# Optimization experiments

Measured on AMD Instinct MI355X. Metric: run time of the kernel, lower is better.

## Reference

```python
import jax, jax.numpy as jnp
import numpy as np

N = 100000
E = 500000
LATENT = 256
EDGE_DIM = 128
HIDDEN = 2 * EDGE_DIM  # 256


def setup_inputs() -> dict:
    key = jax.random.key(0)
    k_z, k_e, k_w1, k_b1, k_w2, k_b2 = jax.random.split(key, 6)
    z = jax.random.normal(k_z, (N, LATENT), dtype=jnp.float32)
    edge_index = jax.random.randint(k_e, (2, E), 0, N, dtype=jnp.int64)
    # torch nn.Linear init: U(-1/sqrt(fan_in), 1/sqrt(fan_in))
    lim1 = 1.0 / np.sqrt(2 * LATENT)
    W1 = jax.random.uniform(k_w1, (HIDDEN, 2 * LATENT), jnp.float32, -lim1, lim1)
    b1 = jax.random.uniform(k_b1, (HIDDEN,), jnp.float32, -lim1, lim1)
    lim2 = 1.0 / np.sqrt(HIDDEN)
    W2 = jax.random.uniform(k_w2, (EDGE_DIM, HIDDEN), jnp.float32, -lim2, lim2)
    b2 = jax.random.uniform(k_b2, (EDGE_DIM,), jnp.float32, -lim2, lim2)
    return {"z": z, "edge_index": edge_index, "W1": W1, "b1": b1, "W2": W2, "b2": b2}


def reference(z, edge_index, W1, b1, W2, b2):
    # Gather endpoint embeddings and concat: [E, 2*latent]
    src = z[edge_index[0]]
    dst = z[edge_index[1]]
    pair = jnp.concatenate([src, dst], axis=1)
    # 2-layer MLP (dropout is identity in eval mode)
    h = jax.nn.relu(pair @ W1.T + b1)
    out = h @ W2.T + b2  # [E, edge_dim]
    return out
```

## Files before the change

kernel.cpp:

```cpp
#include <hip/hip_runtime.h>
#include <hip/hip_bf16.h>

#define N_NODES 100000
#define N_EDGES 500000

typedef __attribute__((ext_vector_type(8))) short  short8;
typedef __attribute__((ext_vector_type(4))) short  short4v;
typedef __attribute__((ext_vector_type(4))) float  float4v;

__device__ __forceinline__ unsigned short f2bf(float f) {
    union { float f; unsigned int u; } v; v.f = f;
    unsigned int u = v.u;
    unsigned int r = u + 0x7fffu + ((u >> 16) & 1u);
    return (unsigned short)(r >> 16);
}
__device__ __forceinline__ float bf2f(unsigned short b) {
    union { unsigned int u; float f; } v; v.u = ((unsigned int)b) << 16;
    return v.f;
}

__device__ __forceinline__ void gload_lds16(const unsigned short* g, unsigned short* l) {
    __builtin_amdgcn_global_load_lds(
        (const __attribute__((address_space(1))) unsigned int*)g,
        (__attribute__((address_space(3))) unsigned int*)l, 16, 0, 0);
}

__global__ void zconv_kernel(const float* __restrict__ z, unsigned short* __restrict__ zb) {
    size_t i = ((size_t)blockIdx.x * 256 + threadIdx.x) * 8;
    float4v a = *(const float4v*)(z + i);
    float4v b = *(const float4v*)(z + i + 4);
    short8 o;
    o[0] = (short)f2bf(a.x); o[1] = (short)f2bf(a.y); o[2] = (short)f2bf(a.z); o[3] = (short)f2bf(a.w);
    o[4] = (short)f2bf(b.x); o[5] = (short)f2bf(b.y); o[6] = (short)f2bf(b.z); o[7] = (short)f2bf(b.w);
    *(short8*)(zb + i) = o;
}

__global__ void prep_kernel(const float* __restrict__ W1, const float* __restrict__ W2,
                            unsigned short* __restrict__ w1c, unsigned short* __restrict__ w2b) {
    int j = blockIdx.x, k = threadIdx.x;
    if (j < 512) {
        float v = (j < 256) ? W1[(size_t)j * 512 + k] : W1[(size_t)(j - 256) * 512 + 256 + k];
        w1c[(size_t)j * 256 + k] = f2bf(v);
    } else {
        int o = j - 512;
        w2b[(size_t)o * 256 + k] = f2bf(W2[(size_t)o * 256 + k]);
    }
}

__launch_bounds__(256, 2)
__global__ void stage1_kernel(const unsigned short* __restrict__ zb,
                              const unsigned short* __restrict__ w1c,
                              unsigned short* __restrict__ ZW) {
    __shared__ unsigned short lds[128 * 136];
    unsigned short* At = lds;
    unsigned short* Bt = lds + 128 * 64;

    const int t    = threadIdx.x;
    const int lane = t & 63, wave = t >> 6;
    const int wm = wave >> 1, wn = wave & 1;
    const int l15 = lane & 15, quad = lane >> 4;
    const int mbase = blockIdx.x * 128, nbase = blockIdx.y * 128;

    const int lr = lane >> 3;
    const int cg = (lane & 7) ^ lr;
    const unsigned short* ag[4]; const unsigned short* bg[4];
    unsigned short* al[4]; unsigned short* bl[4];
#pragma unroll
    for (int q = 0; q < 4; ++q) {
        int rA = wave * 32 + q * 8 + lr;
        int gA = mbase + rA; if (gA >= N_NODES) gA = N_NODES - 1;
        ag[q] = zb  + (size_t)gA * 256 + cg * 8;
        bg[q] = w1c + (size_t)(nbase + rA) * 256 + cg * 8;
        al[q] = At + (wave * 4 + q) * 512 + lane * 8;
        bl[q] = Bt + (wave * 4 + q) * 512 + lane * 8;
    }

    float4v acc[4][4];
    const float4v fz = {0.f, 0.f, 0.f, 0.f};
#pragma unroll
    for (int i = 0; i < 4; ++i)
#pragma unroll
        for (int j = 0; j < 4; ++j) acc[i][j] = fz;

    for (int kk = 0; kk < 256; kk += 64) {
        __syncthreads();
#pragma unroll
        for (int q = 0; q < 4; ++q) gload_lds16(ag[q] + kk, al[q]);
#pragma unroll
        for (int q = 0; q < 4; ++q) gload_lds16(bg[q] + kk, bl[q]);
        __syncthreads();

#pragma unroll
        for (int s = 0; s < 2; ++s) {
            const int ch = ((s * 4 + quad) ^ (l15 & 7)) * 8;
            short8 af[4], bfr[4];
#pragma unroll
            for (int i = 0; i < 4; ++i)
                af[i] = *(const short8*)(At + (wm * 64 + i * 16 + l15) * 64 + ch);
#pragma unroll
            for (int j = 0; j < 4; ++j)
                bfr[j] = *(const short8*)(Bt + (wn * 64 + j * 16 + l15) * 64 + ch);
#pragma unroll
            for (int i = 0; i < 4; ++i)
#pragma unroll
                for (int j = 0; j < 4; ++j)
                    acc[i][j] = __builtin_amdgcn_mfma_f32_16x16x32_bf16(af[i], bfr[j], acc[i][j], 0, 0, 0);
        }
    }

    __syncthreads();
#pragma unroll
    for (int i = 0; i < 4; ++i)
#pragma unroll
        for (int j = 0; j < 4; ++j) {
            int row = wm * 64 + i * 16 + quad * 4;
            int col = wn * 64 + j * 16 + l15;
#pragma unroll
            for (int r = 0; r < 4; ++r)
                lds[(row + r) * 136 + col] = f2bf(acc[i][j][r]);
        }
    __syncthreads();
    for (int c = t; c < 128 * 16; c += 256) {
        int row = c >> 4, ch2 = c & 15;
        int grow = mbase + row;
        if (grow < N_NODES)
            *(short8*)(ZW + (size_t)grow * 512 + nbase + ch2 * 8) =
                *(const short8*)(lds + row * 136 + ch2 * 8);
    }
}

#define H_PITCH 264
#define EBLK 64
__launch_bounds__(256, 4)
__global__ void stage2_kernel(const int* __restrict__ eidx, const unsigned short* __restrict__ ZW,
                              const float* __restrict__ b1, const unsigned short* __restrict__ w2b,
                              const float* __restrict__ b2, float* __restrict__ out) {
    __shared__ unsigned short h[EBLK * H_PITCH];
    __shared__ int idx[128];
    float* hf = (float*)h;
    const int t    = threadIdx.x;
    const int lane = t & 63, wave = t >> 6;
    const int l15 = lane & 15, quad = lane >> 4;
    const int wm = wave >> 1, wn = wave & 1;
    const int eb = blockIdx.x * EBLK;

    if (t < 128) {
        int e = eb + (t & 63); if (e >= N_EDGES) e = N_EDGES - 1;
        idx[t] = eidx[(t >> 6) * N_EDGES + e];
    }
    __syncthreads();

    const int lj = t & 31, er = t >> 5;
    float4v b1a = *(const float4v*)(b1 + lj * 8);
    float4v b1b = *(const float4v*)(b1 + lj * 8 + 4);
    const unsigned short* zs = ZW + lj * 8;
    const unsigned short* zd = ZW + 256 + lj * 8;

    short8 va[8], vb[8];
#pragma unroll
    for (int p = 0; p < 8; ++p) {
        int el = p * 8 + er;
        va[p] = *(const short8*)(zs + (size_t)idx[el] * 512);
        vb[p] = *(const short8*)(zd + (size_t)idx[64 + el] * 512);
    }
#pragma unroll
    for (int p = 0; p < 8; ++p) {
        int el = p * 8 + er;
        short8 xa = va[p], xb = vb[p];
        short8 rv;
#pragma unroll
        for (int i = 0; i < 8; ++i) {
            float v = bf2f((unsigned short)xa[i]) + bf2f((unsigned short)xb[i])
                    + ((i < 4) ? b1a[i] : b1b[i - 4]);
            v = v > 0.f ? v : 0.f;
            rv[i] = (short)f2bf(v);
        }
        *(short8*)(h + el * H_PITCH + lj * 8) = rv;
    }
    __syncthreads();

    const unsigned short* wr[4];
#pragma unroll
    for (int j = 0; j < 4; ++j)
        wr[j] = w2b + (size_t)(wn * 64 + j * 16 + l15) * 256 + quad * 8;

    float4v acc[2][4];
    const float4v fz = {0.f, 0.f, 0.f, 0.f};
#pragma unroll
    for (int i = 0; i < 2; ++i)
#pragma unroll
        for (int j = 0; j < 4; ++j) acc[i][j] = fz;

    short8 pre[4][2];
#pragma unroll
    for (int kk = 0; kk < 2; ++kk)
#pragma unroll
        for (int j = 0; j < 4; ++j) pre[j][kk] = *(const short8*)(wr[j] + kk * 32);

#pragma unroll
    for (int kk = 0; kk < 8; ++kk) {
        short8 af[2];
#pragma unroll
        for (int i = 0; i < 2; ++i)
            af[i] = *(const short8*)(h + (wm * 32 + i * 16 + l15) * H_PITCH + kk * 32 + quad * 8);
        short8 bcur[4];
#pragma unroll
        for (int j = 0; j < 4; ++j) bcur[j] = pre[j][kk & 1];
        if (kk < 6) {
#pragma unroll
            for (int j = 0; j < 4; ++j) pre[j][kk & 1] = *(const short8*)(wr[j] + (kk + 2) * 32);
        }
#pragma unroll
        for (int i = 0; i < 2; ++i)
#pragma unroll
            for (int j = 0; j < 4; ++j)
                acc[i][j] = __builtin_amdgcn_mfma_f32_16x16x32_bf16(af[i], bcur[j], acc[i][j], 0, 0, 0);
    }

    __syncthreads();
#pragma unroll
    for (int j = 0; j < 4; ++j) {
        int col = wn * 64 + j * 16 + l15;
        float bias = b2[col];
#pragma unroll
        for (int i = 0; i < 2; ++i) {
            int row0 = wm * 32 + i * 16 + quad * 4;
#pragma unroll
            for (int r = 0; r < 4; ++r)
                hf[(row0 + r) * 132 + col] = acc[i][j][r] + bias;
        }
    }
    __syncthreads();
#pragma unroll
    for (int pass = 0; pass < 8; ++pass) {
        int it  = pass * 256 + t;
        int row = it >> 5, c4 = (it & 31) * 4;
        int e = eb + row;
        if (e < N_EDGES) {
            float4v v = *(const float4v*)(hf + row * 132 + c4);
            __builtin_nontemporal_store(v, (float4v*)(out + (size_t)e * 128 + c4));
        }
    }
}

__global__ void fallback_kernel(const float* __restrict__ z, const int* __restrict__ eidx,
                                const float* __restrict__ W1, const float* __restrict__ b1,
                                const float* __restrict__ W2, const float* __restrict__ b2,
                                float* __restrict__ out) {
    __shared__ float zs[512];
    __shared__ float hh[256];
    int e = blockIdx.x, t = threadIdx.x;
    int s = eidx[e], d = eidx[N_EDGES + e];
    zs[t]       = z[(size_t)s * 256 + t];
    zs[256 + t] = z[(size_t)d * 256 + t];
    __syncthreads();
    float a = b1[t];
    const float* wr = W1 + (size_t)t * 512;
    for (int k = 0; k < 512; ++k) a += zs[k] * wr[k];
    hh[t] = a > 0.f ? a : 0.f;
    __syncthreads();
    if (t < 128) {
        float o = b2[t];
        const float* w2r = W2 + (size_t)t * 256;
        for (int k = 0; k < 256; ++k) o += hh[k] * w2r[k];
        out[(size_t)e * 128 + t] = o;
    }
}

extern "C" void kernel_launch(void* const* d_in, const int* in_sizes, int n_in,
                              void* d_out, int out_size, void* d_ws, size_t ws_size,
                              hipStream_t stream) {
    const float* z    = (const float*)d_in[0];
    const int*   eidx = (const int*)d_in[1];
    const float* W1   = (const float*)d_in[2];
    const float* b1   = (const float*)d_in[3];
    const float* W2   = (const float*)d_in[4];
    const float* b2   = (const float*)d_in[5];
    float* out = (float*)d_out;

    const size_t zw_bytes = (size_t)N_NODES * 512 * 2;
    const size_t w1c_off  = zw_bytes;
    const size_t w2b_off  = w1c_off + (size_t)512 * 256 * 2;
    const size_t need     = w2b_off + (size_t)128 * 256 * 2;

    if (ws_size < need) {
        fallback_kernel<<<N_EDGES, 256, 0, stream>>>(z, eidx, W1, b1, W2, b2, out);
        return;
    }
    unsigned short* ZW  = (unsigned short*)d_ws;
    unsigned short* w1c = (unsigned short*)((char*)d_ws + w1c_off);
    unsigned short* w2b = (unsigned short*)((char*)d_ws + w2b_off);
    unsigned short* zb  = (unsigned short*)d_out;

    zconv_kernel<<<12500, 256, 0, stream>>>(z, zb);
    prep_kernel<<<640, 256, 0, stream>>>(W1, W2, w1c, w2b);
    stage1_kernel<<<dim3(782, 4), 256, 0, stream>>>(zb, w1c, ZW);
    stage2_kernel<<<(N_EDGES + EBLK - 1) / EBLK, 256, 0, stream>>>(eidx, ZW, b1, w2b, b2, out);
}
```

Before: 486.7 us.

## Make stage2 persistent over edge tiles with prefetched gathers and register-resident W2

```diff
diff --git a/kernel.cpp b/kernel.cpp
--- a/kernel.cpp
+++ b/kernel.cpp
@@ -130,116 +130,123 @@
 }
 
 #define H_PITCH 264
-#define EBLK 64
-__launch_bounds__(256, 4)
+#define EBLK 32
+#define NT 8
+__launch_bounds__(256, 3)
 __global__ void stage2_kernel(const int* __restrict__ eidx, const unsigned short* __restrict__ ZW,
                               const float* __restrict__ b1, const unsigned short* __restrict__ w2b,
                               const float* __restrict__ b2, float* __restrict__ out) {
     __shared__ unsigned short h[EBLK * H_PITCH];
-    __shared__ int idx[128];
+    __shared__ int idx2[512];
     float* hf = (float*)h;
+
     const int t    = threadIdx.x;
     const int lane = t & 63, wave = t >> 6;
+    const int lj = lane & 31, hi = lane >> 5;
     const int l15 = lane & 15, quad = lane >> 4;
-    const int wm = wave >> 1, wn = wave & 1;
-    const int eb = blockIdx.x * EBLK;
-
-    if (t < 128) {
-        int e = eb + (t & 63); if (e >= N_EDGES) e = N_EDGES - 1;
-        idx[t] = eidx[(t >> 6) * N_EDGES + e];
-    }
-    __syncthreads();
-
-    const int lj = t & 31, er = t >> 5;
+    const int w8 = wave * 8;
+    const int eb0 = blockIdx.x * (EBLK * NT);
+
+    {
+        int e = eb0 + t; if (e >= N_EDGES) e = N_EDGES - 1;
+        idx2[t]       = eidx[e];
+        idx2[256 + t] = eidx[N_EDGES + e];
+    }
+    __syncthreads();
+
+    short8 bfrag[2][8];
+#pragma unroll
+    for (int jj = 0; jj < 2; ++jj)
+#pragma unroll
+        for (int kk = 0; kk < 8; ++kk)
+            bfrag[jj][kk] = *(const short8*)(w2b + (size_t)(wave * 32 + jj * 16 + l15) * 256
+                                             + kk * 32 + quad * 8);
+
     float4v b1a = *(const float4v*)(b1 + lj * 8);
     float4v b1b = *(const float4v*)(b1 + lj * 8 + 4);
+    float b2r[2];
+#pragma unroll
+    for (int jj = 0; jj < 2; ++jj) b2r[jj] = b2[wave * 32 + jj * 16 + l15];
     const unsigned short* zs = ZW + lj * 8;
     const unsigned short* zd = ZW + 256 + lj * 8;
 
-    short8 va[8], vb[8];
-#pragma unroll
-    for (int p = 0; p < 8; ++p) {
-        int el = p * 8 + er;
-        va[p] = *(const short8*)(zs + (size_t)idx[el] * 512);
-        vb[p] = *(const short8*)(zd + (size_t)idx[64 + el] * 512);
-    }
-#pragma unroll
-    for (int p = 0; p < 8; ++p) {
-        int el = p * 8 + er;
-        short8 xa = va[p], xb = vb[p];
-        short8 rv;
-#pragma unroll
-        for (int i = 0; i < 8; ++i) {
-            float v = bf2f((unsigned short)xa[i]) + bf2f((unsigned short)xb[i])
-                    + ((i < 4) ? b1a[i] : b1b[i - 4]);
-            v = v > 0.f ? v : 0.f;
-            rv[i] = (short)f2bf(v);
-        }
-        *(short8*)(h + el * H_PITCH + lj * 8) = rv;
-    }
-    __syncthreads();
-
-    const unsigned short* wr[4];
-#pragma unroll
-    for (int j = 0; j < 4; ++j)
-        wr[j] = w2b + (size_t)(wn * 64 + j * 16 + l15) * 256 + quad * 8;
-
-    float4v acc[2][4];
-    const float4v fz = {0.f, 0.f, 0.f, 0.f};
-#pragma unroll
-    for (int i = 0; i < 2; ++i)
-#pragma unroll
-        for (int j = 0; j < 4; ++j) acc[i][j] = fz;
-
-    short8 pre[4][2];
-#pragma unroll
-    for (int kk = 0; kk < 2; ++kk)
-#pragma unroll
-        for (int j = 0; j < 4; ++j) pre[j][kk] = *(const short8*)(wr[j] + kk * 32);
-
-#pragma unroll
-    for (int kk = 0; kk < 8; ++kk) {
-        short8 af[2];
-#pragma unroll
-        for (int i = 0; i < 2; ++i)
-            af[i] = *(const short8*)(h + (wm * 32 + i * 16 + l15) * H_PITCH + kk * 32 + quad * 8);
-        short8 bcur[4];
-#pragma unroll
-        for (int j = 0; j < 4; ++j) bcur[j] = pre[j][kk & 1];
-        if (kk < 6) {
-#pragma unroll
-            for (int j = 0; j < 4; ++j) pre[j][kk & 1] = *(const short8*)(wr[j] + (kk + 2) * 32);
-        }
-#pragma unroll
-        for (int i = 0; i < 2; ++i)
-#pragma unroll
-            for (int j = 0; j < 4; ++j)
-                acc[i][j] = __builtin_amdgcn_mfma_f32_16x16x32_bf16(af[i], bcur[j], acc[i][j], 0, 0, 0);
-    }
-
-    __syncthreads();
-#pragma unroll
-    for (int j = 0; j < 4; ++j) {
-        int col = wn * 64 + j * 16 + l15;
-        float bias = b2[col];
-#pragma unroll
-        for (int i = 0; i < 2; ++i) {
-            int row0 = wm * 32 + i * 16 + quad * 4;
-#pragma unroll
-            for (int r = 0; r < 4; ++r)
-                hf[(row0 + r) * 132 + col] = acc[i][j][r] + bias;
-        }
-    }
-    __syncthreads();
-#pragma unroll
-    for (int pass = 0; pass < 8; ++pass) {
-        int it  = pass * 256 + t;
-        int row = it >> 5, c4 = (it & 31) * 4;
-        int e = eb + row;
-        if (e < N_EDGES) {
-            float4v v = *(const float4v*)(hf + row * 132 + c4);
-            __builtin_nontemporal_store(v, (float4v*)(out + (size_t)e * 128 + c4));
-        }
+    short8 va[4], vb[4];
+#pragma unroll
+    for (int p = 0; p < 4; ++p) {
+        int r = w8 + p * 2 + hi;
+        va[p] = *(const short8*)(zs + (size_t)idx2[r] * 512);
+        vb[p] = *(const short8*)(zd + (size_t)idx2[256 + r] * 512);
+    }
+    __builtin_amdgcn_sched_barrier(0);
+
+    for (int tt = 0; tt < NT; ++tt) {
+        const int tb = tt * 32;
+#pragma unroll
+        for (int p = 0; p < 4; ++p) {
+            int r = w8 + p * 2 + hi;
+            short8 xa = va[p], xb = vb[p];
+            short8 rv;
+#pragma unroll
+            for (int i = 0; i < 8; ++i) {
+                float v = bf2f((unsigned short)xa[i]) + bf2f((unsigned short)xb[i])
+                        + ((i < 4) ? b1a[i] : b1b[i - 4]);
+                v = v > 0.f ? v : 0.f;
+                rv[i] = (short)f2bf(v);
+            }
+            *(short8*)(h + r * H_PITCH + lj * 8) = rv;
+        }
+        if (tt + 1 < NT) {
+            const int tb2 = tb + 32;
+#pragma unroll
+            for (int p = 0; p < 4; ++p) {
+                int r = tb2 + w8 + p * 2 + hi;
+                va[p] = *(const short8*)(zs + (size_t)idx2[r] * 512);
+                vb[p] = *(const short8*)(zd + (size_t)idx2[256 + r] * 512);
+            }
+        }
+        __builtin_amdgcn_sched_barrier(0);
+        asm volatile("s_waitcnt lgkmcnt(0)" ::: "memory");
+        __builtin_amdgcn_s_barrier();
+        __builtin_amdgcn_sched_barrier(0);
+        float4v acc[2][2];
+        const float4v fz = {0.f, 0.f, 0.f, 0.f};
+        acc[0][0] = fz; acc[0][1] = fz; acc[1][0] = fz; acc[1][1] = fz;
+#pragma unroll
+        for (int kk = 0; kk < 8; ++kk) {
+            short8 af0 = *(const short8*)(h + (l15)      * H_PITCH + kk * 32 + quad * 8);
+            short8 af1 = *(const short8*)(h + (16 + l15) * H_PITCH + kk * 32 + quad * 8);
+            acc[0][0] = __builtin_amdgcn_mfma_f32_16x16x32_bf16(af0, bfrag[0][kk], acc[0][0], 0, 0, 0);
+            acc[0][1] = __builtin_amdgcn_mfma_f32_16x16x32_bf16(af0, bfrag[1][kk], acc[0][1], 0, 0, 0);
+            acc[1][0] = __builtin_amdgcn_mfma_f32_16x16x32_bf16(af1, bfrag[0][kk], acc[1][0], 0, 0, 0);
+            acc[1][1] = __builtin_amdgcn_mfma_f32_16x16x32_bf16(af1, bfrag[1][kk], acc[1][1], 0, 0, 0);
+        }
+        __builtin_amdgcn_sched_barrier(0);
+        __builtin_amdgcn_s_barrier();
+        __builtin_amdgcn_sched_barrier(0);
+#pragma unroll
+        for (int jj = 0; jj < 2; ++jj)
+#pragma unroll
+            for (int i = 0; i < 2; ++i)
+#pragma unroll
+                for (int r = 0; r < 4; ++r)
+                    hf[(i * 16 + quad * 4 + r) * 132 + wave * 32 + jj * 16 + l15] =
+                        acc[i][jj][r] + b2r[jj];
+        asm volatile("s_waitcnt lgkmcnt(0)" ::: "memory");
+        __builtin_amdgcn_s_barrier();
+        __builtin_amdgcn_sched_barrier(0);
+#pragma unroll
+        for (int pass = 0; pass < 4; ++pass) {
+            int it = pass * 256 + t;
+            int row = it >> 5, c4 = (it & 31) * 4;
+            int e = eb0 + tb + row;
+            if (e < N_EDGES) {
+                float4v v = *(const float4v*)(hf + row * 132 + c4);
+                __builtin_nontemporal_store(v, (float4v*)(out + (size_t)e * 128 + c4));
+            }
+        }
+        __builtin_amdgcn_sched_barrier(0);
+        __builtin_amdgcn_s_barrier();
+        __builtin_amdgcn_sched_barrier(0);
     }
 }
 
@@ -295,5 +302,6 @@
     zconv_kernel<<<12500, 256, 0, stream>>>(z, zb);
     prep_kernel<<<640, 256, 0, stream>>>(W1, W2, w1c, w2b);
     stage1_kernel<<<dim3(782, 4), 256, 0, stream>>>(zb, w1c, ZW);
-    stage2_kernel<<<(N_EDGES + EBLK - 1) / EBLK, 256, 0, stream>>>(eidx, ZW, b1, w2b, b2, out);
-}
+    const int s2_blocks = (N_EDGES + EBLK * NT - 1) / (EBLK * NT);
+    stage2_kernel<<<s2_blocks, 256, 0, stream>>>(eidx, ZW, b1, w2b, b2, out);
+}
```

Result: faster. 448.3 us (-7.9%).
